# Kernel optimization log

Measured on AMD Instinct MI355X. Metric: run time of the kernel, lower is better.

Reference implementation:

```python
import jax, jax.numpy as jnp
import numpy as np

ATTN_MULT = 8.0
NEG_INF = float('-inf')

N, Q, S, D = 16, 2048, 2048, 64


def setup_inputs() -> dict:
    key = jax.random.key(0)
    kq, kk, kv, kp = jax.random.split(key, 4)
    return {
        "queries_nqd": jax.random.normal(kq, (N, Q, D), dtype=jnp.float32),
        "keys_nsd": jax.random.normal(kk, (N, S, D), dtype=jnp.float32),
        "values_nsv": jax.random.normal(kv, (N, S, D), dtype=jnp.float32),
        "prefix_len_n": jax.random.randint(kp, (N,), 0, S, dtype=jnp.int64 if jax.config.jax_enable_x64 else jnp.int32),
    }


def reference(queries_nqd, keys_nsd, values_nsv, prefix_len_n):
    # attention_type == 'block_diagonal', backend == 'torch', dropout p == 0
    n, q, d = queries_nqd.shape
    s = keys_nsd.shape[1]
    scale = ATTN_MULT / d
    # prefix-block mask: key position < prefix_len (broadcast over queries)
    block_mask_n1s = (jnp.arange(s)[None, None, :] < prefix_len_n[:, None, None])  # [n,1,s]
    diag_mask_qs = jnp.arange(q)[:, None] == jnp.arange(s)[None, :]                # [q,s]
    mask_nqs = block_mask_n1s | diag_mask_qs[None, :, :]                           # [n,q,s]
    scores_nqs = jnp.einsum('nqd,nsd->nqs', queries_nqd, keys_nsd) * scale
    scores_nqs = jnp.where(mask_nqs, scores_nqs, NEG_INF)
    probs_nqs = jax.nn.softmax(scores_nqs, axis=-1)
    return jnp.einsum('nqs,nsv->nqv', probs_nqs, values_nsv)
```

## Files before the change

### kernel.cpp

```cpp
#include <hip/hip_runtime.h>
#include <math.h>

#define NH 16
#define QL 2048
#define SL 2048
#define DD 64
#define PSTR 72
#define QK_SCALE_LOG2E 0.1803368801111f

typedef __attribute__((ext_vector_type(8))) short short8;
typedef __attribute__((ext_vector_type(4))) float floatx4;
typedef __attribute__((ext_vector_type(4))) unsigned short ushort4v;
typedef __attribute__((ext_vector_type(8))) unsigned short ushort8v;

__device__ __forceinline__ unsigned short f2bf(float x) {
    unsigned u = __float_as_uint(x);
    u += 0x7FFFu + ((u >> 16) & 1u);
    return (unsigned short)(u >> 16);
}

__device__ __forceinline__ void gld16(const unsigned short* g, unsigned short* l) {
    __builtin_amdgcn_global_load_lds(
        (const __attribute__((address_space(1))) unsigned int*)g,
        (__attribute__((address_space(3))) unsigned int*)l, 16, 0, 0);
}

__global__ __launch_bounds__(256) void convqk(
    const float* __restrict__ Qf, const float* __restrict__ Kf,
    unsigned short* __restrict__ Qb, unsigned short* __restrict__ Kb)
{
    int idx = blockIdx.x * 256 + threadIdx.x;
    const float4* src; unsigned short* dst; float scale;
    if (blockIdx.y == 0) { src = (const float4*)Qf; dst = Qb; scale = QK_SCALE_LOG2E; }
    else                 { src = (const float4*)Kf; dst = Kb; scale = 1.0f; }
    float4 v = src[idx];
    ushort4v h = { f2bf(v.x * scale), f2bf(v.y * scale), f2bf(v.z * scale), f2bf(v.w * scale) };
    *(ushort4v*)(dst + (size_t)idx * 4) = h;
}

__global__ __launch_bounds__(256) void transv(
    const float* __restrict__ Vf, unsigned short* __restrict__ Vtb)
{
    __shared__ unsigned short sT[64][PSTR];
    int bx = blockIdx.x;
    int n = bx >> 5, stile = bx & 31, s0 = stile * 64;
    int tid = (int)threadIdx.x;
    const float* vb = Vf + ((size_t)n * SL + s0) * DD;
    #pragma unroll
    for (int i = 0; i < 4; ++i) {
        int idx = tid + i * 256;
        int r = idx >> 4, c = (idx & 15) << 2;
        float4 v = *(const float4*)(vb + r * DD + c);
        sT[c + 0][r] = f2bf(v.x);
        sT[c + 1][r] = f2bf(v.y);
        sT[c + 2][r] = f2bf(v.z);
        sT[c + 3][r] = f2bf(v.w);
    }
    __syncthreads();
    int d = tid >> 2, sg = tid & 3;
    unsigned short* out = Vtb + (size_t)n * DD * SL + (size_t)d * SL + s0 + sg * 16;
    ushort8v a, b;
    #pragma unroll
    for (int i = 0; i < 8; ++i) { a[i] = sT[d][sg * 16 + i]; b[i] = sT[d][sg * 16 + 8 + i]; }
    *(ushort8v*)(out) = a;
    *(ushort8v*)(out + 8) = b;
}

__global__ __launch_bounds__(256, 3) void attn_mfma_split(
    const unsigned short* __restrict__ Qb, const unsigned short* __restrict__ Kb,
    const unsigned short* __restrict__ Vtb, const int* __restrict__ plen_g,
    float* __restrict__ Op, float* __restrict__ Lp, int spl)
{
    __shared__ unsigned short sQ[64 * 64];
    __shared__ unsigned short sK[2][64 * 64];
    __shared__ unsigned short sVt[2][64 * 64];
    __shared__ unsigned short sP[4 * 16 * PSTR];

    const int blk = blockIdx.x;
    const int n  = blk & (NH - 1);
    const int qt = blk >> 4;
    const int q0 = qt * 64;
    const int sp = blockIdx.y;
    const int sbeg = sp * spl;
    const int plen = plen_g[n];
    const int ntile = spl >> 6;
    const bool hasdiag = (q0 >= sbeg) && (q0 < sbeg + spl);
    if (!((sbeg < plen) || hasdiag)) return;

    const int tid  = (int)threadIdx.x;
    const int wave = tid >> 6, lane = tid & 63, quad = lane >> 4, l16 = lane & 15;

    int rem  = plen - sbeg;
    int base = (rem > 0) ? min((rem + 63) >> 6, ntile) : 0;
    int td   = hasdiag ? ((q0 - sbeg) >> 6) : -1;
    int total = base + ((td >= base) ? 1 : 0);

    const unsigned short* kh = Kb  + (size_t)n * SL * DD;
    const unsigned short* vh = Vtb + (size_t)n * DD * SL;

    const int seg0 = wave * 2, seg1 = wave * 2 + 1;
    const int r0 = seg0 * 8 + (lane >> 3), r1 = seg1 * 8 + (lane >> 3);
    const int cg0 = ((lane & 7) ^ (r0 & 7)) * 8, cg1 = ((lane & 7) ^ (r1 & 7)) * 8;

    {
        const unsigned short* qg = Qb + ((size_t)(n * QL + q0)) * DD;
        gld16(qg + r0 * DD + cg0, sQ + seg0 * 512);
        gld16(qg + r1 * DD + cg1, sQ + seg1 * 512);
        int t0 = (0 < base) ? 0 : td;
        const unsigned short* kg = kh + (size_t)(sbeg + t0 * 64) * DD;
        const unsigned short* vg = vh + (sbeg + t0 * 64);
        gld16(kg + r0 * DD + cg0, sK[0] + seg0 * 512);
        gld16(kg + r1 * DD + cg1, sK[0] + seg1 * 512);
        gld16(vg + (size_t)r0 * SL + cg0, sVt[0] + seg0 * 512);
        gld16(vg + (size_t)r1 * SL + cg1, sVt[0] + seg1 * 512);
    }

    floatx4 acc[4];
    #pragma unroll
    for (int dt = 0; dt < 4; ++dt) acc[dt] = (floatx4){0.f, 0.f, 0.f, 0.f};
    float lsum = 0.f;

    const int qrow = wave * 16 + l16;
    short8 bQ0, bQ1;

    for (int i = 0; i < total; ++i) {
        __syncthreads();

        if (i + 1 < total) {
            int tn = (i + 1 < base) ? (i + 1) : td;
            const unsigned short* kg = kh + (size_t)(sbeg + tn * 64) * DD;
            const unsigned short* vg = vh + (sbeg + tn * 64);
            unsigned short* dk = sK[(i + 1) & 1];
            unsigned short* dv = sVt[(i + 1) & 1];
            gld16(kg + r0 * DD + cg0, dk + seg0 * 512);
            gld16(kg + r1 * DD + cg1, dk + seg1 * 512);
            gld16(vg + (size_t)r0 * SL + cg0, dv + seg0 * 512);
            gld16(vg + (size_t)r1 * SL + cg1, dv + seg1 * 512);
        }
        if (i == 0) {
            bQ0 = *(const short8*)(sQ + qrow * 64 + (((0 * 4 + quad) ^ (qrow & 7)) * 8));
            bQ1 = *(const short8*)(sQ + qrow * 64 + (((1 * 4 + quad) ^ (qrow & 7)) * 8));
        }

        const unsigned short* sk = sK[i & 1];
        const unsigned short* sv = sVt[i & 1];
        const int t  = (i < base) ? i : td;
        const int s0 = sbeg + t * 64;

        floatx4 sf[4];
        #pragma unroll
        for (int st2 = 0; st2 < 4; ++st2) sf[st2] = (floatx4){0.f, 0.f, 0.f, 0.f};
        #pragma unroll
        for (int st2 = 0; st2 < 4; ++st2) {
            int krow = st2 * 16 + l16;
            short8 aK0 = *(const short8*)(sk + krow * 64 + (((0 * 4 + quad) ^ (krow & 7)) * 8));
            short8 aK1 = *(const short8*)(sk + krow * 64 + (((1 * 4 + quad) ^ (krow & 7)) * 8));
            sf[st2] = __builtin_amdgcn_mfma_f32_16x16x32_bf16(aK0, bQ0, sf[st2], 0, 0, 0);
            sf[st2] = __builtin_amdgcn_mfma_f32_16x16x32_bf16(aK1, bQ1, sf[st2], 0, 0, 0);
        }

        const int qcol = q0 + qrow;
        unsigned short* pw = sP + qrow * PSTR;
        if (s0 + 64 <= plen) {
            #pragma unroll
            for (int st2 = 0; st2 < 4; ++st2) {
                float p0 = __builtin_amdgcn_exp2f(sf[st2][0]);
                float p1 = __builtin_amdgcn_exp2f(sf[st2][1]);
                float p2 = __builtin_amdgcn_exp2f(sf[st2][2]);
                float p3 = __builtin_amdgcn_exp2f(sf[st2][3]);
                lsum += (p0 + p1) + (p2 + p3);
                ushort4v pk = { f2bf(p0), f2bf(p1), f2bf(p2), f2bf(p3) };
                *(ushort4v*)(pw + st2 * 16 + quad * 4) = pk;
            }
        } else {
            #pragma unroll
            for (int st2 = 0; st2 < 4; ++st2) {
                float p[4];
                #pragma unroll
                for (int r = 0; r < 4; ++r) {
                    int s = s0 + st2 * 16 + quad * 4 + r;
                    bool valid = (s < plen) || (s == qcol);
                    p[r] = __builtin_amdgcn_exp2f(valid ? sf[st2][r] : -INFINITY);
                    lsum += p[r];
                }
                ushort4v pk = { f2bf(p[0]), f2bf(p[1]), f2bf(p[2]), f2bf(p[3]) };
                *(ushort4v*)(pw + st2 * 16 + quad * 4) = pk;
            }
        }

        #pragma unroll
        for (int ks = 0; ks < 2; ++ks) {
            short8 aP = *(const short8*)(sP + qrow * PSTR + ks * 32 + quad * 8);
            #pragma unroll
            for (int dt = 0; dt < 4; ++dt) {
                int vrow = dt * 16 + l16;
                short8 bV = *(const short8*)(sv + vrow * 64 + (((ks * 4 + quad) ^ (vrow & 7)) * 8));
                acc[dt] = __builtin_amdgcn_mfma_f32_16x16x32_bf16(aP, bV, acc[dt], 0, 0, 0);
            }
        }
    }

    lsum += __shfl_xor(lsum, 16, 64);
    lsum += __shfl_xor(lsum, 32, 64);
    if (quad == 0)
        Lp[((size_t)sp * NH + n) * QL + q0 + qrow] = lsum;

    float* ob = Op + (((size_t)sp * NH + n) * QL + q0) * DD;
    #pragma unroll
    for (int r = 0; r < 4; ++r) {
        int ql = wave * 16 + quad * 4 + r;
        #pragma unroll
        for (int dt = 0; dt < 4; ++dt)
            ob[(size_t)ql * DD + dt * 16 + l16] = acc[dt][r];
    }
}

__global__ __launch_bounds__(256) void combine(
    const float* __restrict__ Op, const float* __restrict__ Lp,
    const int* __restrict__ plen_g, float* __restrict__ Og, int nsplit, int spl)
{
    int idx = blockIdx.x * 256 + (int)threadIdx.x;
    int d4 = idx & 15;
    int q  = (idx >> 4) & (QL - 1);
    int n  = idx >> 15;
    int plen = plen_g[n];
    int spd = q / spl;
    float4 s = {0.f, 0.f, 0.f, 0.f};
    float l = 0.f;
    for (int sp = 0; sp < nsplit; ++sp) {
        if ((sp * spl < plen) || (sp == spd)) {
            const float* ob = Op + (((size_t)sp * NH + n) * QL + q) * DD;
            float4 v = *(const float4*)(ob + d4 * 4);
            s.x += v.x; s.y += v.y; s.z += v.z; s.w += v.w;
            l += Lp[((size_t)sp * NH + n) * QL + q];
        }
    }
    float inv = 1.0f / l;
    float4 o = { s.x * inv, s.y * inv, s.z * inv, s.w * inv };
    *(float4*)(Og + ((size_t)n * QL + q) * DD + d4 * 4) = o;
}

extern "C" void kernel_launch(void* const* d_in, const int* in_sizes, int n_in,
                              void* d_out, int out_size, void* d_ws, size_t ws_size,
                              hipStream_t stream) {
    const float* Qf   = (const float*)d_in[0];
    const float* Kf   = (const float*)d_in[1];
    const float* Vf   = (const float*)d_in[2];
    const int*   plen = (const int*)d_in[3];
    float* Og = (float*)d_out;

    char* ws = (char*)d_ws;
    unsigned short* Qb  = (unsigned short*)(ws);
    unsigned short* Kb  = (unsigned short*)(ws + (4u << 20));
    unsigned short* Vtb = (unsigned short*)(ws + (8u << 20));
    float* Op = (float*)(ws + (12u << 20));

    const size_t op_bytes = (size_t)NH * QL * DD * 4;
    const size_t lp_bytes = (size_t)NH * QL * 4;
    int nsplit = 1;
    if (ws_size >= (12u << 20) + 4 * (op_bytes + lp_bytes)) nsplit = 4;
    else if (ws_size >= (12u << 20) + 2 * (op_bytes + lp_bytes)) nsplit = 2;
    float* Lp = (float*)(ws + (12u << 20) + (size_t)nsplit * op_bytes);
    int spl = SL / nsplit;

    convqk<<<dim3(2048, 2), 256, 0, stream>>>(Qf, Kf, Qb, Kb);
    transv<<<512, 256, 0, stream>>>(Vf, Vtb);
    attn_mfma_split<<<dim3(NH * (QL / 64), nsplit), 256, 0, stream>>>(Qb, Kb, Vtb, plen, Op, Lp, spl);
    combine<<<2048, 256, 0, stream>>>(Op, Lp, plen, Og, nsplit, spl);
}
```

Before: 114.6 us.

## Load K/V fragments directly from global into registers and merge prep kernels

The attention kernel no longer stages K and V^T tiles through double-buffered LDS with global_load_lds and per-tile barriers. Each wave now loads its MFMA K and V operand fragments straight from global memory into registers, and Q fragments are loaded once at the start. The Q/K conversion and V transpose kernels are merged into one launch to save a launch. The risk is that each of the four waves loads the same K/V tile separately, so global/L2 traffic rises, and the loads are not prefetched ahead of use, so their latency may stall the MFMAs.

```diff
diff --git a/kernel.cpp b/kernel.cpp
--- a/kernel.cpp
+++ b/kernel.cpp
@@ -19,61 +19,51 @@
     return (unsigned short)(u >> 16);
 }
 
-__device__ __forceinline__ void gld16(const unsigned short* g, unsigned short* l) {
-    __builtin_amdgcn_global_load_lds(
-        (const __attribute__((address_space(1))) unsigned int*)g,
-        (__attribute__((address_space(3))) unsigned int*)l, 16, 0, 0);
-}
-
-__global__ __launch_bounds__(256) void convqk(
-    const float* __restrict__ Qf, const float* __restrict__ Kf,
-    unsigned short* __restrict__ Qb, unsigned short* __restrict__ Kb)
+__global__ __launch_bounds__(256) void prep(
+    const float* __restrict__ Qf, const float* __restrict__ Kf, const float* __restrict__ Vf,
+    unsigned short* __restrict__ Qb, unsigned short* __restrict__ Kb, unsigned short* __restrict__ Vtb)
 {
-    int idx = blockIdx.x * 256 + threadIdx.x;
-    const float4* src; unsigned short* dst; float scale;
-    if (blockIdx.y == 0) { src = (const float4*)Qf; dst = Qb; scale = QK_SCALE_LOG2E; }
-    else                 { src = (const float4*)Kf; dst = Kb; scale = 1.0f; }
-    float4 v = src[idx];
-    ushort4v h = { f2bf(v.x * scale), f2bf(v.y * scale), f2bf(v.z * scale), f2bf(v.w * scale) };
-    *(ushort4v*)(dst + (size_t)idx * 4) = h;
-}
-
-__global__ __launch_bounds__(256) void transv(
-    const float* __restrict__ Vf, unsigned short* __restrict__ Vtb)
-{
-    __shared__ unsigned short sT[64][PSTR];
-    int bx = blockIdx.x;
-    int n = bx >> 5, stile = bx & 31, s0 = stile * 64;
-    int tid = (int)threadIdx.x;
-    const float* vb = Vf + ((size_t)n * SL + s0) * DD;
-    #pragma unroll
-    for (int i = 0; i < 4; ++i) {
-        int idx = tid + i * 256;
-        int r = idx >> 4, c = (idx & 15) << 2;
-        float4 v = *(const float4*)(vb + r * DD + c);
-        sT[c + 0][r] = f2bf(v.x);
-        sT[c + 1][r] = f2bf(v.y);
-        sT[c + 2][r] = f2bf(v.z);
-        sT[c + 3][r] = f2bf(v.w);
-    }
-    __syncthreads();
-    int d = tid >> 2, sg = tid & 3;
-    unsigned short* out = Vtb + (size_t)n * DD * SL + (size_t)d * SL + s0 + sg * 16;
-    ushort8v a, b;
-    #pragma unroll
-    for (int i = 0; i < 8; ++i) { a[i] = sT[d][sg * 16 + i]; b[i] = sT[d][sg * 16 + 8 + i]; }
-    *(ushort8v*)(out) = a;
-    *(ushort8v*)(out + 8) = b;
-}
-
-__global__ __launch_bounds__(256, 3) void attn_mfma_split(
+    if (blockIdx.y < 2) {
+        int idx = blockIdx.x * 256 + threadIdx.x;
+        const float4* src; unsigned short* dst; float scale;
+        if (blockIdx.y == 0) { src = (const float4*)Qf; dst = Qb; scale = QK_SCALE_LOG2E; }
+        else                 { src = (const float4*)Kf; dst = Kb; scale = 1.0f; }
+        float4 v = src[idx];
+        ushort4v h = { f2bf(v.x * scale), f2bf(v.y * scale), f2bf(v.z * scale), f2bf(v.w * scale) };
+        *(ushort4v*)(dst + (size_t)idx * 4) = h;
+    } else {
+        if (blockIdx.x >= 512) return;
+        __shared__ unsigned short sT[64][PSTR];
+        int bx = blockIdx.x;
+        int n = bx >> 5, stile = bx & 31, s0 = stile * 64;
+        int tid = (int)threadIdx.x;
+        const float* vb = Vf + ((size_t)n * SL + s0) * DD;
+        #pragma unroll
+        for (int i = 0; i < 4; ++i) {
+            int idx = tid + i * 256;
+            int r = idx >> 4, c = (idx & 15) << 2;
+            float4 v = *(const float4*)(vb + r * DD + c);
+            sT[c + 0][r] = f2bf(v.x);
+            sT[c + 1][r] = f2bf(v.y);
+            sT[c + 2][r] = f2bf(v.z);
+            sT[c + 3][r] = f2bf(v.w);
+        }
+        __syncthreads();
+        int d = tid >> 2, sg = tid & 3;
+        unsigned short* out = Vtb + (size_t)n * DD * SL + (size_t)d * SL + s0 + sg * 16;
+        ushort8v a, b;
+        #pragma unroll
+        for (int i = 0; i < 8; ++i) { a[i] = sT[d][sg * 16 + i]; b[i] = sT[d][sg * 16 + 8 + i]; }
+        *(ushort8v*)(out) = a;
+        *(ushort8v*)(out + 8) = b;
+    }
+}
+
+__global__ __launch_bounds__(256, 3) void attn_mfma_reg(
     const unsigned short* __restrict__ Qb, const unsigned short* __restrict__ Kb,
     const unsigned short* __restrict__ Vtb, const int* __restrict__ plen_g,
     float* __restrict__ Op, float* __restrict__ Lp, int spl)
 {
-    __shared__ unsigned short sQ[64 * 64];
-    __shared__ unsigned short sK[2][64 * 64];
-    __shared__ unsigned short sVt[2][64 * 64];
     __shared__ unsigned short sP[4 * 16 * PSTR];
 
     const int blk = blockIdx.x;
@@ -95,72 +85,49 @@
     int td   = hasdiag ? ((q0 - sbeg) >> 6) : -1;
     int total = base + ((td >= base) ? 1 : 0);
 
+    const int qrow  = wave * 16 + l16;
+    const int qglob = q0 + qrow;
+
+    const unsigned short* qg = Qb + ((size_t)(n * QL + qglob)) * DD + quad * 8;
+    short8 bQ0 = *(const short8*)(qg);
+    short8 bQ1 = *(const short8*)(qg + 32);
+
     const unsigned short* kh = Kb  + (size_t)n * SL * DD;
     const unsigned short* vh = Vtb + (size_t)n * DD * SL;
-
-    const int seg0 = wave * 2, seg1 = wave * 2 + 1;
-    const int r0 = seg0 * 8 + (lane >> 3), r1 = seg1 * 8 + (lane >> 3);
-    const int cg0 = ((lane & 7) ^ (r0 & 7)) * 8, cg1 = ((lane & 7) ^ (r1 & 7)) * 8;
-
-    {
-        const unsigned short* qg = Qb + ((size_t)(n * QL + q0)) * DD;
-        gld16(qg + r0 * DD + cg0, sQ + seg0 * 512);
-        gld16(qg + r1 * DD + cg1, sQ + seg1 * 512);
-        int t0 = (0 < base) ? 0 : td;
-        const unsigned short* kg = kh + (size_t)(sbeg + t0 * 64) * DD;
-        const unsigned short* vg = vh + (sbeg + t0 * 64);
-        gld16(kg + r0 * DD + cg0, sK[0] + seg0 * 512);
-        gld16(kg + r1 * DD + cg1, sK[0] + seg1 * 512);
-        gld16(vg + (size_t)r0 * SL + cg0, sVt[0] + seg0 * 512);
-        gld16(vg + (size_t)r1 * SL + cg1, sVt[0] + seg1 * 512);
-    }
 
     floatx4 acc[4];
     #pragma unroll
     for (int dt = 0; dt < 4; ++dt) acc[dt] = (floatx4){0.f, 0.f, 0.f, 0.f};
     float lsum = 0.f;
-
-    const int qrow = wave * 16 + l16;
-    short8 bQ0, bQ1;
+    unsigned short* pw = sP + qrow * PSTR;
 
     for (int i = 0; i < total; ++i) {
-        __syncthreads();
-
-        if (i + 1 < total) {
-            int tn = (i + 1 < base) ? (i + 1) : td;
-            const unsigned short* kg = kh + (size_t)(sbeg + tn * 64) * DD;
-            const unsigned short* vg = vh + (sbeg + tn * 64);
-            unsigned short* dk = sK[(i + 1) & 1];
-            unsigned short* dv = sVt[(i + 1) & 1];
-            gld16(kg + r0 * DD + cg0, dk + seg0 * 512);
-            gld16(kg + r1 * DD + cg1, dk + seg1 * 512);
-            gld16(vg + (size_t)r0 * SL + cg0, dv + seg0 * 512);
-            gld16(vg + (size_t)r1 * SL + cg1, dv + seg1 * 512);
-        }
-        if (i == 0) {
-            bQ0 = *(const short8*)(sQ + qrow * 64 + (((0 * 4 + quad) ^ (qrow & 7)) * 8));
-            bQ1 = *(const short8*)(sQ + qrow * 64 + (((1 * 4 + quad) ^ (qrow & 7)) * 8));
-        }
-
-        const unsigned short* sk = sK[i & 1];
-        const unsigned short* sv = sVt[i & 1];
         const int t  = (i < base) ? i : td;
         const int s0 = sbeg + t * 64;
 
+        const unsigned short* kt = kh + ((size_t)(s0 + l16)) * DD + quad * 8;
+        short8 aK[4][2];
+        #pragma unroll
+        for (int st2 = 0; st2 < 4; ++st2) {
+            aK[st2][0] = *(const short8*)(kt + (size_t)st2 * 16 * DD);
+            aK[st2][1] = *(const short8*)(kt + (size_t)st2 * 16 * DD + 32);
+        }
+        const unsigned short* vt = vh + (size_t)l16 * SL + s0 + quad * 8;
+        short8 bV[4][2];
+        #pragma unroll
+        for (int dt = 0; dt < 4; ++dt) {
+            bV[dt][0] = *(const short8*)(vt + (size_t)dt * 16 * SL);
+            bV[dt][1] = *(const short8*)(vt + (size_t)dt * 16 * SL + 32);
+        }
+
         floatx4 sf[4];
         #pragma unroll
-        for (int st2 = 0; st2 < 4; ++st2) sf[st2] = (floatx4){0.f, 0.f, 0.f, 0.f};
-        #pragma unroll
         for (int st2 = 0; st2 < 4; ++st2) {
-            int krow = st2 * 16 + l16;
-            short8 aK0 = *(const short8*)(sk + krow * 64 + (((0 * 4 + quad) ^ (krow & 7)) * 8));
-            short8 aK1 = *(const short8*)(sk + krow * 64 + (((1 * 4 + quad) ^ (krow & 7)) * 8));
-            sf[st2] = __builtin_amdgcn_mfma_f32_16x16x32_bf16(aK0, bQ0, sf[st2], 0, 0, 0);
-            sf[st2] = __builtin_amdgcn_mfma_f32_16x16x32_bf16(aK1, bQ1, sf[st2], 0, 0, 0);
-        }
-
-        const int qcol = q0 + qrow;
-        unsigned short* pw = sP + qrow * PSTR;
+            sf[st2] = (floatx4){0.f, 0.f, 0.f, 0.f};
+            sf[st2] = __builtin_amdgcn_mfma_f32_16x16x32_bf16(aK[st2][0], bQ0, sf[st2], 0, 0, 0);
+            sf[st2] = __builtin_amdgcn_mfma_f32_16x16x32_bf16(aK[st2][1], bQ1, sf[st2], 0, 0, 0);
+        }
+
         if (s0 + 64 <= plen) {
             #pragma unroll
             for (int st2 = 0; st2 < 4; ++st2) {
@@ -179,7 +146,7 @@
                 #pragma unroll
                 for (int r = 0; r < 4; ++r) {
                     int s = s0 + st2 * 16 + quad * 4 + r;
-                    bool valid = (s < plen) || (s == qcol);
+                    bool valid = (s < plen) || (s == qglob);
                     p[r] = __builtin_amdgcn_exp2f(valid ? sf[st2][r] : -INFINITY);
                     lsum += p[r];
                 }
@@ -192,11 +159,8 @@
         for (int ks = 0; ks < 2; ++ks) {
             short8 aP = *(const short8*)(sP + qrow * PSTR + ks * 32 + quad * 8);
             #pragma unroll
-            for (int dt = 0; dt < 4; ++dt) {
-                int vrow = dt * 16 + l16;
-                short8 bV = *(const short8*)(sv + vrow * 64 + (((ks * 4 + quad) ^ (vrow & 7)) * 8));
-                acc[dt] = __builtin_amdgcn_mfma_f32_16x16x32_bf16(aP, bV, acc[dt], 0, 0, 0);
-            }
+            for (int dt = 0; dt < 4; ++dt)
+                acc[dt] = __builtin_amdgcn_mfma_f32_16x16x32_bf16(aP, bV[dt][ks], acc[dt], 0, 0, 0);
         }
     }
 
@@ -263,8 +227,7 @@
     float* Lp = (float*)(ws + (12u << 20) + (size_t)nsplit * op_bytes);
     int spl = SL / nsplit;
 
-    convqk<<<dim3(2048, 2), 256, 0, stream>>>(Qf, Kf, Qb, Kb);
-    transv<<<512, 256, 0, stream>>>(Vf, Vtb);
-    attn_mfma_split<<<dim3(NH * (QL / 64), nsplit), 256, 0, stream>>>(Qb, Kb, Vtb, plen, Op, Lp, spl);
+    prep<<<dim3(2048, 3), 256, 0, stream>>>(Qf, Kf, Vf, Qb, Kb, Vtb);
+    attn_mfma_reg<<<dim3(NH * (QL / 64), nsplit), 256, 0, stream>>>(Qb, Kb, Vtb, plen, Op, Lp, spl);
     combine<<<2048, 256, 0, stream>>>(Op, Lp, plen, Og, nsplit, spl);
 }
```

Result: slower. 192.1 us (+67.7%).

## Merge prep kernels, drop Q shared tile, swizzle P buffer for higher occupancy

Applied to the files above, without the earlier changes.

Folds the Q/K conversion and V transpose into one prep launch, which removes a kernel launch. The attention kernel no longer stages Q in LDS and instead loads each lane's Q fragment straight from global memory. The P scratch buffer loses its padding and uses an XOR swizzle to avoid bank conflicts. Together these cut LDS use, so launch bounds are raised to four blocks per CU. The cost is that the prep grid now has 1536 idle V blocks that exit immediately.

```diff
diff --git a/kernel.cpp b/kernel.cpp
--- a/kernel.cpp
+++ b/kernel.cpp
@@ -25,56 +25,54 @@
         (__attribute__((address_space(3))) unsigned int*)l, 16, 0, 0);
 }
 
-__global__ __launch_bounds__(256) void convqk(
-    const float* __restrict__ Qf, const float* __restrict__ Kf,
-    unsigned short* __restrict__ Qb, unsigned short* __restrict__ Kb)
+__global__ __launch_bounds__(256) void prep(
+    const float* __restrict__ Qf, const float* __restrict__ Kf, const float* __restrict__ Vf,
+    unsigned short* __restrict__ Qb, unsigned short* __restrict__ Kb, unsigned short* __restrict__ Vtb)
 {
-    int idx = blockIdx.x * 256 + threadIdx.x;
-    const float4* src; unsigned short* dst; float scale;
-    if (blockIdx.y == 0) { src = (const float4*)Qf; dst = Qb; scale = QK_SCALE_LOG2E; }
-    else                 { src = (const float4*)Kf; dst = Kb; scale = 1.0f; }
-    float4 v = src[idx];
-    ushort4v h = { f2bf(v.x * scale), f2bf(v.y * scale), f2bf(v.z * scale), f2bf(v.w * scale) };
-    *(ushort4v*)(dst + (size_t)idx * 4) = h;
-}
-
-__global__ __launch_bounds__(256) void transv(
-    const float* __restrict__ Vf, unsigned short* __restrict__ Vtb)
-{
-    __shared__ unsigned short sT[64][PSTR];
-    int bx = blockIdx.x;
-    int n = bx >> 5, stile = bx & 31, s0 = stile * 64;
-    int tid = (int)threadIdx.x;
-    const float* vb = Vf + ((size_t)n * SL + s0) * DD;
-    #pragma unroll
-    for (int i = 0; i < 4; ++i) {
-        int idx = tid + i * 256;
-        int r = idx >> 4, c = (idx & 15) << 2;
-        float4 v = *(const float4*)(vb + r * DD + c);
-        sT[c + 0][r] = f2bf(v.x);
-        sT[c + 1][r] = f2bf(v.y);
-        sT[c + 2][r] = f2bf(v.z);
-        sT[c + 3][r] = f2bf(v.w);
-    }
-    __syncthreads();
-    int d = tid >> 2, sg = tid & 3;
-    unsigned short* out = Vtb + (size_t)n * DD * SL + (size_t)d * SL + s0 + sg * 16;
-    ushort8v a, b;
-    #pragma unroll
-    for (int i = 0; i < 8; ++i) { a[i] = sT[d][sg * 16 + i]; b[i] = sT[d][sg * 16 + 8 + i]; }
-    *(ushort8v*)(out) = a;
-    *(ushort8v*)(out + 8) = b;
-}
-
-__global__ __launch_bounds__(256, 3) void attn_mfma_split(
+    if (blockIdx.y < 2) {
+        int idx = blockIdx.x * 256 + threadIdx.x;
+        const float4* src; unsigned short* dst; float scale;
+        if (blockIdx.y == 0) { src = (const float4*)Qf; dst = Qb; scale = QK_SCALE_LOG2E; }
+        else                 { src = (const float4*)Kf; dst = Kb; scale = 1.0f; }
+        float4 v = src[idx];
+        ushort4v h = { f2bf(v.x * scale), f2bf(v.y * scale), f2bf(v.z * scale), f2bf(v.w * scale) };
+        *(ushort4v*)(dst + (size_t)idx * 4) = h;
+    } else {
+        if (blockIdx.x >= 512) return;
+        __shared__ unsigned short sT[64][PSTR];
+        int bx = blockIdx.x;
+        int n = bx >> 5, stile = bx & 31, s0 = stile * 64;
+        int tid = (int)threadIdx.x;
+        const float* vb = Vf + ((size_t)n * SL + s0) * DD;
+        #pragma unroll
+        for (int i = 0; i < 4; ++i) {
+            int idx = tid + i * 256;
+            int r = idx >> 4, c = (idx & 15) << 2;
+            float4 v = *(const float4*)(vb + r * DD + c);
+            sT[c + 0][r] = f2bf(v.x);
+            sT[c + 1][r] = f2bf(v.y);
+            sT[c + 2][r] = f2bf(v.z);
+            sT[c + 3][r] = f2bf(v.w);
+        }
+        __syncthreads();
+        int d = tid >> 2, sg = tid & 3;
+        unsigned short* out = Vtb + (size_t)n * DD * SL + (size_t)d * SL + s0 + sg * 16;
+        ushort8v a, b;
+        #pragma unroll
+        for (int i = 0; i < 8; ++i) { a[i] = sT[d][sg * 16 + i]; b[i] = sT[d][sg * 16 + 8 + i]; }
+        *(ushort8v*)(out) = a;
+        *(ushort8v*)(out + 8) = b;
+    }
+}
+
+__global__ __launch_bounds__(256, 4) void attn_mfma_split(
     const unsigned short* __restrict__ Qb, const unsigned short* __restrict__ Kb,
     const unsigned short* __restrict__ Vtb, const int* __restrict__ plen_g,
     float* __restrict__ Op, float* __restrict__ Lp, int spl)
 {
-    __shared__ unsigned short sQ[64 * 64];
     __shared__ unsigned short sK[2][64 * 64];
     __shared__ unsigned short sVt[2][64 * 64];
-    __shared__ unsigned short sP[4 * 16 * PSTR];
+    __shared__ unsigned short sP[4 * 16 * 64];
 
     const int blk = blockIdx.x;
     const int n  = blk & (NH - 1);
@@ -95,6 +93,14 @@
     int td   = hasdiag ? ((q0 - sbeg) >> 6) : -1;
     int total = base + ((td >= base) ? 1 : 0);
 
+    const int qrow  = wave * 16 + l16;
+    const int qglob = q0 + qrow;
+    const int pmask = (l16 & 7) * 8;
+
+    const unsigned short* qg = Qb + ((size_t)(n * QL + qglob)) * DD + quad * 8;
+    short8 bQ0 = *(const short8*)(qg);
+    short8 bQ1 = *(const short8*)(qg + 32);
+
     const unsigned short* kh = Kb  + (size_t)n * SL * DD;
     const unsigned short* vh = Vtb + (size_t)n * DD * SL;
 
@@ -103,9 +109,6 @@
     const int cg0 = ((lane & 7) ^ (r0 & 7)) * 8, cg1 = ((lane & 7) ^ (r1 & 7)) * 8;
 
     {
-        const unsigned short* qg = Qb + ((size_t)(n * QL + q0)) * DD;
-        gld16(qg + r0 * DD + cg0, sQ + seg0 * 512);
-        gld16(qg + r1 * DD + cg1, sQ + seg1 * 512);
         int t0 = (0 < base) ? 0 : td;
         const unsigned short* kg = kh + (size_t)(sbeg + t0 * 64) * DD;
         const unsigned short* vg = vh + (sbeg + t0 * 64);
@@ -119,9 +122,7 @@
     #pragma unroll
     for (int dt = 0; dt < 4; ++dt) acc[dt] = (floatx4){0.f, 0.f, 0.f, 0.f};
     float lsum = 0.f;
-
-    const int qrow = wave * 16 + l16;
-    short8 bQ0, bQ1;
+    unsigned short* pw = sP + qrow * 64;
 
     for (int i = 0; i < total; ++i) {
         __syncthreads();
@@ -137,10 +138,6 @@
             gld16(vg + (size_t)r0 * SL + cg0, dv + seg0 * 512);
             gld16(vg + (size_t)r1 * SL + cg1, dv + seg1 * 512);
         }
-        if (i == 0) {
-            bQ0 = *(const short8*)(sQ + qrow * 64 + (((0 * 4 + quad) ^ (qrow & 7)) * 8));
-            bQ1 = *(const short8*)(sQ + qrow * 64 + (((1 * 4 + quad) ^ (qrow & 7)) * 8));
-        }
 
         const unsigned short* sk = sK[i & 1];
         const unsigned short* sv = sVt[i & 1];
@@ -159,8 +156,6 @@
             sf[st2] = __builtin_amdgcn_mfma_f32_16x16x32_bf16(aK1, bQ1, sf[st2], 0, 0, 0);
         }
 
-        const int qcol = q0 + qrow;
-        unsigned short* pw = sP + qrow * PSTR;
         if (s0 + 64 <= plen) {
             #pragma unroll
             for (int st2 = 0; st2 < 4; ++st2) {
@@ -170,7 +165,7 @@
                 float p3 = __builtin_amdgcn_exp2f(sf[st2][3]);
                 lsum += (p0 + p1) + (p2 + p3);
                 ushort4v pk = { f2bf(p0), f2bf(p1), f2bf(p2), f2bf(p3) };
-                *(ushort4v*)(pw + st2 * 16 + quad * 4) = pk;
+                *(ushort4v*)(pw + ((st2 * 16 + quad * 4) ^ pmask)) = pk;
             }
         } else {
             #pragma unroll
@@ -179,18 +174,18 @@
                 #pragma unroll
                 for (int r = 0; r < 4; ++r) {
                     int s = s0 + st2 * 16 + quad * 4 + r;
-                    bool valid = (s < plen) || (s == qcol);
+                    bool valid = (s < plen) || (s == qglob);
                     p[r] = __builtin_amdgcn_exp2f(valid ? sf[st2][r] : -INFINITY);
                     lsum += p[r];
                 }
                 ushort4v pk = { f2bf(p[0]), f2bf(p[1]), f2bf(p[2]), f2bf(p[3]) };
-                *(ushort4v*)(pw + st2 * 16 + quad * 4) = pk;
+                *(ushort4v*)(pw + ((st2 * 16 + quad * 4) ^ pmask)) = pk;
             }
         }
 
         #pragma unroll
         for (int ks = 0; ks < 2; ++ks) {
-            short8 aP = *(const short8*)(sP + qrow * PSTR + ks * 32 + quad * 8);
+            short8 aP = *(const short8*)(pw + ((ks * 32 + quad * 8) ^ pmask));
             #pragma unroll
             for (int dt = 0; dt < 4; ++dt) {
                 int vrow = dt * 16 + l16;
@@ -263,8 +258,7 @@
     float* Lp = (float*)(ws + (12u << 20) + (size_t)nsplit * op_bytes);
     int spl = SL / nsplit;
 
-    convqk<<<dim3(2048, 2), 256, 0, stream>>>(Qf, Kf, Qb, Kb);
-    transv<<<512, 256, 0, stream>>>(Vf, Vtb);
+    prep<<<dim3(2048, 3), 256, 0, stream>>>(Qf, Kf, Vf, Qb, Kb, Vtb);
     attn_mfma_split<<<dim3(NH * (QL / 64), nsplit), 256, 0, stream>>>(Qb, Kb, Vtb, plen, Op, Lp, spl);
     combine<<<2048, 256, 0, stream>>>(Op, Lp, plen, Og, nsplit, spl);
 }
```

New measurement: 111.8 us. -2.4%, faster.
